# Kernel optimization log

Hardware: AMD Instinct MI355X
Metric: run time of the kernel (lower is better)

The kernel has to match this reference:

```python
import jax, jax.numpy as jnp
import numpy as np

D = 256      # d_model
A = 64       # attn_dim
K = 16       # k_neighbors
N = 20000    # embedding table rows
B = 32768    # batch of perturbed genes
SCALE = A ** -0.5
EPS = 1e-5


def setup_inputs() -> dict:
    key = jax.random.key(0)
    ks = jax.random.split(key, 12)
    all_embs = jax.random.normal(ks[0], (N, D), dtype=jnp.float32)
    center_idx = jax.random.randint(ks[1], (B,), 0, N)
    nb_idx = jax.random.randint(ks[2], (B, K), 0, N)
    nb_weights = jax.random.uniform(ks[3], (B, K), dtype=jnp.float32)
    # learned params (torch Linear weight layout: [out, in])
    s = lambda fan_in: 1.0 / np.sqrt(fan_in)
    Wq = jax.random.uniform(ks[4], (A, D), minval=-s(D), maxval=s(D))
    Wk = jax.random.uniform(ks[5], (A, D), minval=-s(D), maxval=s(D))
    Wg = jax.random.uniform(ks[6], (D, D), minval=-s(D), maxval=s(D))
    bg = jax.random.uniform(ks[7], (D,), minval=-s(D), maxval=s(D))
    Wo = jax.random.uniform(ks[8], (D, 2 * D), minval=-s(2 * D), maxval=s(2 * D))
    bo = jax.random.uniform(ks[9], (D,), minval=-s(2 * D), maxval=s(2 * D))
    gamma = jnp.ones((D,), jnp.float32)
    beta = jnp.zeros((D,), jnp.float32)
    return dict(all_embs=all_embs, center_idx=center_idx, nb_idx=nb_idx,
                nb_weights=nb_weights, Wq=Wq, Wk=Wk, Wg=Wg, bg=bg,
                Wo=Wo, bo=bo, gamma=gamma, beta=beta)


def reference(all_embs, center_idx, nb_idx, nb_weights, Wq, Wk, Wg, bg, Wo, bo, gamma, beta):
    center = all_embs[center_idx]                      # [B, D]
    nbs = all_embs[nb_idx]                             # [B, K, D]
    q = center @ Wq.T                                  # [B, A]
    k = jnp.einsum('bkd,ad->bka', nbs, Wk)             # [B, K, A]
    logits = jnp.einsum('ba,bka->bk', q, k) * SCALE
    logits = logits + jnp.log(jnp.clip(nb_weights, 1e-6))
    attn = jax.nn.softmax(logits, axis=-1)             # [B, K]
    gate = jax.nn.sigmoid(center @ Wg.T + bg)          # [B, D]
    context = gate * jnp.einsum('bk,bkd->bd', attn, nbs)
    combined = jnp.concatenate([center, context], axis=-1)  # [B, 2D]
    enriched = combined @ Wo.T + bo                    # [B, D]
    x = enriched + center
    mu = jnp.mean(x, axis=-1, keepdims=True)
    var = jnp.var(x, axis=-1, keepdims=True)
    return (x - mu) * jax.lax.rsqrt(var + EPS) * gamma + beta
```

## Files before the change

### kernel.cpp

```cpp
#include <hip/hip_runtime.h>

#define DD 256
#define MM 16

typedef __attribute__((ext_vector_type(8))) short bfrag;
typedef __attribute__((ext_vector_type(4))) float ffrag;

__device__ __forceinline__ float lo2f(unsigned int p){ union{unsigned int i; float f;} v; v.i = p<<16; return v.f; }
__device__ __forceinline__ float hi2f(unsigned int p){ union{unsigned int i; float f;} v; v.i = p & 0xffff0000u; return v.f; }
__device__ __forceinline__ float bf2f(unsigned short u){ union{unsigned int i; float f;} v; v.i = ((unsigned int)u)<<16; return v.f; }
__device__ __forceinline__ unsigned short f2b(float x){
    union{float f; unsigned int i;} v; v.f = x;
    unsigned int r = v.i + 0x7fffu + ((v.i>>16)&1u);
    return (unsigned short)(r>>16);
}
__device__ __forceinline__ unsigned int pack2(float a, float b){
    return (unsigned int)f2b(a) | ((unsigned int)f2b(b)<<16);
}

__device__ __forceinline__ int swz256(int d, int e){
    return ((d>>4)*8 + (e>>5))*512 + (((e>>3)&3)*16 + (d&15))*8 + (e&7);
}
__device__ __forceinline__ int swz512(int d, int e){
    return ((d>>4)*16 + (e>>5))*512 + (((e>>3)&3)*16 + (d&15))*8 + (e&7);
}

extern "C" __global__ __launch_bounds__(256)
void prep_all(const float* __restrict__ Wq, const float* __restrict__ Wk,
              const float* __restrict__ Wg, const float* __restrict__ Wo,
              const float* __restrict__ embs, unsigned short* __restrict__ ws, int n8)
{
    int bid = blockIdx.x, e = threadIdx.x;
    if (bid < 256) {
        int d = bid; float acc = 0.f;
        #pragma unroll 8
        for (int a = 0; a < 64; ++a) acc = fmaf(Wq[a*256 + e], Wk[a*256 + d], acc);
        ws[swz256(d, e)] = f2b(acc);
    } else if (bid < 512) {
        int r = bid - 256;
        ws[65536 + swz256(r, e)] = f2b(Wg[r*256 + e]);
    } else if (bid < 768) {
        int r = bid - 512;
        ws[131072 + swz512(r, e)]       = f2b(Wo[r*512 + e]);
        ws[131072 + swz512(r, e + 256)] = f2b(Wo[r*512 + 256 + e]);
    } else {
        int i = (bid - 768)*256 + e;
        if (i < n8) {
            const float4* s = (const float4*)embs + (size_t)i*2;
            float4 a = s[0], b = s[1];
            uint4 o;
            o.x = pack2(a.x,a.y); o.y = pack2(a.z,a.w);
            o.z = pack2(b.x,b.y); o.w = pack2(b.z,b.w);
            ((uint4*)(ws + 262144))[i] = o;
        }
    }
}

template<bool TBF>
__device__ __forceinline__ void gather8(uint4* buf, const unsigned short* tbl,
                                        const float* embs, int idx, int p)
{
    if (TBF) {
        const unsigned short* base = tbl + (size_t)idx*DD + p*8;
        #pragma unroll
        for (int i = 0; i < 8; ++i) buf[i] = *(const uint4*)(base + i*32);
    } else {
        const float* base = embs + (size_t)idx*DD + p*8;
        #pragma unroll
        for (int i = 0; i < 8; ++i) {
            float4 a = *(const float4*)(base + i*32);
            float4 b = *(const float4*)(base + i*32 + 4);
            buf[i].x = pack2(a.x,a.y); buf[i].y = pack2(a.z,a.w);
            buf[i].z = pack2(b.x,b.y); buf[i].w = pack2(b.z,b.w);
        }
    }
}

template<bool TBF>
__global__ __launch_bounds__(256, 3)
void na_mfma9(const float* __restrict__ embs,
              const int* __restrict__ cidx,
              const int* __restrict__ nidx,
              const float* __restrict__ nbw,
              const unsigned short* __restrict__ tbl,
              const unsigned short* __restrict__ wMt,
              const unsigned short* __restrict__ wWg,
              const unsigned short* __restrict__ wWo,
              const float* __restrict__ bg,
              const float* __restrict__ bo,
              const float* __restrict__ gamma,
              const float* __restrict__ beta,
              float* __restrict__ out)
{
    __shared__ __align__(16) unsigned short s_ax[16][264];
    __shared__ __align__(16) unsigned short s_t[16][264];
    __shared__ __align__(16) unsigned short s_nb[4][16][264];
    __shared__ float s_attn[4][16];
    __shared__ int   s_cidx[16];
    float* s_x = (float*)&s_nb[0][0][0];

    const int tid  = threadIdx.x;
    const int row0 = blockIdx.x * MM;
    const int lane = tid & 63, wv = tid >> 6;
    const int l15  = lane & 15, quad = lane >> 4;
    const ffrag fz = {0.f, 0.f, 0.f, 0.f};

    if (tid < 16) s_cidx[tid] = cidx[row0 + tid];
    uint4 careg[8];
    {
        int aidx = cidx[row0 + l15];
        if (TBF) {
            const unsigned short* pc = tbl + (size_t)aidx*DD + quad*8;
            #pragma unroll
            for (int kc = 0; kc < 8; ++kc) careg[kc] = *(const uint4*)(pc + kc*32);
        } else {
            const float* pc = embs + (size_t)aidx*DD + quad*8;
            #pragma unroll
            for (int kc = 0; kc < 8; ++kc) {
                float4 a = *(const float4*)(pc + kc*32);
                float4 b = *(const float4*)(pc + kc*32 + 4);
                careg[kc].x = pack2(a.x,a.y); careg[kc].y = pack2(a.z,a.w);
                careg[kc].z = pack2(b.x,b.y); careg[kc].w = pack2(b.z,b.w);
            }
        }
    }

    {
        ffrag at[4] = {fz,fz,fz,fz}, ag[4] = {fz,fz,fz,fz};
        const unsigned short* btA = wMt + (size_t)(wv*4)*4096 + lane*8;
        const unsigned short* bgA = wWg + (size_t)(wv*4)*4096 + lane*8;
        #pragma unroll
        for (int kc = 0; kc < 8; ++kc) {
            bfrag af = *(const bfrag*)&careg[kc];
            #pragma unroll
            for (int t = 0; t < 4; ++t) {
                at[t] = __builtin_amdgcn_mfma_f32_16x16x32_bf16(af, *(const bfrag*)(btA + (size_t)t*4096 + kc*512), at[t], 0,0,0);
                ag[t] = __builtin_amdgcn_mfma_f32_16x16x32_bf16(af, *(const bfrag*)(bgA + (size_t)t*4096 + kc*512), ag[t], 0,0,0);
            }
        }
        #pragma unroll
        for (int t = 0; t < 4; ++t) {
            int col = wv*64 + t*16 + l15;
            float bgv = bg[col];
            #pragma unroll
            for (int r = 0; r < 4; ++r) {
                int rr = quad*4 + r;
                s_t[rr][col]  = f2b(at[t][r]);
                float g = 1.f / (1.f + __expf(-(ag[t][r] + bgv)));
                s_ax[rr][col] = f2b(g);
            }
        }
    }
    __syncthreads();

    {
        const int kn = lane >> 2;
        const int p  = lane & 3;
        int idxs[4];
        #pragma unroll
        for (int j = 0; j < 4; ++j)
            idxs[j] = nidx[(size_t)(row0 + 4*wv + j) * 16 + kn];

        uint4 buf[2][8];
        gather8<TBF>(buf[0], tbl, embs, idxs[0], p);

        #pragma unroll
        for (int j = 0; j < 4; ++j) {
            if (j < 3) gather8<TBF>(buf[(j+1)&1], tbl, embs, idxs[j+1], p);
            const int m = 4*wv + j;
            unsigned short* nbp = &s_nb[wv][kn][p*8];
            #pragma unroll
            for (int i = 0; i < 8; ++i) *(uint4*)(nbp + i*32) = buf[j&1][i];

            const unsigned short* anb  = &s_nb[wv][l15][quad*8];
            const unsigned short* trow = &s_t[m][quad*8];
            ffrag lac = fz;
            #pragma unroll
            for (int kc = 0; kc < 8; ++kc)
                lac = __builtin_amdgcn_mfma_f32_16x16x32_bf16(
                        *(const bfrag*)(anb + kc*32), *(const bfrag*)(trow + kc*32), lac, 0,0,0);

            float4 w4 = *(const float4*)(nbw + (size_t)(row0 + m)*16 + quad*4);
            float lg0 = lac[0]*0.125f, lg1 = lac[1]*0.125f;
            float lg2 = lac[2]*0.125f, lg3 = lac[3]*0.125f;
            float mx = fmaxf(fmaxf(lg0, lg1), fmaxf(lg2, lg3));
            mx = fmaxf(mx, __shfl_xor(mx, 16));
            mx = fmaxf(mx, __shfl_xor(mx, 32));
            float e0 = fmaxf(w4.x, 1e-6f) * __expf(lg0 - mx);
            float e1 = fmaxf(w4.y, 1e-6f) * __expf(lg1 - mx);
            float e2 = fmaxf(w4.z, 1e-6f) * __expf(lg2 - mx);
            float e3 = fmaxf(w4.w, 1e-6f) * __expf(lg3 - mx);
            float s = e0 + e1 + e2 + e3;
            s += __shfl_xor(s, 16); s += __shfl_xor(s, 32);
            float inv = 1.f / s;
            if (l15 == 0)
                *(float4*)&s_attn[wv][quad*4] = make_float4(e0*inv, e1*inv, e2*inv, e3*inv);

            float4 aw0 = *(const float4*)&s_attn[wv][0];
            float4 aw1 = *(const float4*)&s_attn[wv][4];
            float4 aw2 = *(const float4*)&s_attn[wv][8];
            float4 aw3 = *(const float4*)&s_attn[wv][12];
            float aarr[16] = {aw0.x,aw0.y,aw0.z,aw0.w, aw1.x,aw1.y,aw1.z,aw1.w,
                              aw2.x,aw2.y,aw2.z,aw2.w, aw3.x,aw3.y,aw3.z,aw3.w};
            float c0=0.f, c1=0.f, c2=0.f, c3=0.f;
            #pragma unroll
            for (int kk = 0; kk < 16; ++kk) {
                uint2 v = *(const uint2*)&s_nb[wv][kk][lane*4];
                float a = aarr[kk];
                c0 += a * lo2f(v.x); c1 += a * hi2f(v.x);
                c2 += a * lo2f(v.y); c3 += a * hi2f(v.y);
            }
            uint2 g = *(const uint2*)&s_ax[m][lane*4];
            c0 *= lo2f(g.x); c1 *= hi2f(g.x); c2 *= lo2f(g.y); c3 *= hi2f(g.y);
            uint2 o; o.x = pack2(c0, c1); o.y = pack2(c2, c3);
            *(uint2*)&s_ax[m][lane*4] = o;
        }
    }
    __syncthreads();

    {
        ffrag acc[4] = {fz,fz,fz,fz};
        const unsigned short* arx = &s_ax[l15][quad * 8];
        const unsigned short* bO  = wWo + (size_t)(wv*4)*8192 + lane*8;
        #pragma unroll
        for (int kc = 0; kc < 8; ++kc) {
            bfrag af = *(const bfrag*)&careg[kc];
            #pragma unroll
            for (int t = 0; t < 4; ++t)
                acc[t] = __builtin_amdgcn_mfma_f32_16x16x32_bf16(af, *(const bfrag*)(bO + (size_t)t*8192 + kc*512), acc[t], 0,0,0);
        }
        #pragma unroll
        for (int kc = 8; kc < 16; ++kc) {
            bfrag af = *(const bfrag*)(arx + (kc-8)*32);
            #pragma unroll
            for (int t = 0; t < 4; ++t)
                acc[t] = __builtin_amdgcn_mfma_f32_16x16x32_bf16(af, *(const bfrag*)(bO + (size_t)t*8192 + kc*512), acc[t], 0,0,0);
        }
        #pragma unroll
        for (int t = 0; t < 4; ++t) {
            int col = wv*64 + t*16 + l15;
            float bov = bo[col];
            #pragma unroll
            for (int r = 0; r < 4; ++r) {
                int rr = quad*4 + r;
                float ctr = embs[(size_t)s_cidx[rr] * DD + col];
                s_x[rr*260 + col] = acc[t][r] + bov + ctr;
            }
        }
    }
    __syncthreads();

    {
        #pragma unroll
        for (int jj = 0; jj < 4; ++jj) {
            int m = wv * 4 + jj;
            const float* xr = s_x + m*260;
            float x0 = xr[lane],       x1 = xr[64 + lane];
            float x2 = xr[128 + lane], x3 = xr[192 + lane];
            float s  = x0 + x1 + x2 + x3;
            float ss = x0*x0 + x1*x1 + x2*x2 + x3*x3;
            #pragma unroll
            for (int off = 32; off >= 1; off >>= 1) {
                s  += __shfl_xor(s, off);
                ss += __shfl_xor(ss, off);
            }
            float mu  = s * (1.f/256.f);
            float var = ss * (1.f/256.f) - mu*mu;
            float rs  = rsqrtf(var + 1e-5f);
            size_t base = (size_t)(row0 + m) * DD;
            float xs[4] = {x0, x1, x2, x3};
            #pragma unroll
            for (int cc = 0; cc < 4; ++cc) {
                int dd = cc*64 + lane;
                out[base + dd] = (xs[cc] - mu) * rs * gamma[dd] + beta[dd];
            }
        }
    }
}

#define SD 260
#define KT 16
#define WS 17
extern "C" __global__ __launch_bounds__(256)
void na_f32_kernel(const float* __restrict__ embs, const int* __restrict__ center_idx,
                   const int* __restrict__ nb_idx, const float* __restrict__ nb_w,
                   const float* __restrict__ Wq, const float* __restrict__ Wk,
                   const float* __restrict__ Wg, const float* __restrict__ bg,
                   const float* __restrict__ Wo, const float* __restrict__ bo,
                   const float* __restrict__ gamma, const float* __restrict__ beta,
                   float* __restrict__ out)
{
    __shared__ __align__(16) float s_center[MM][SD];
    __shared__ __align__(16) float s_tc[MM][SD];
    __shared__ __align__(16) float s_nb[16][SD];
    __shared__ __align__(16) float s_w[DD][WS];
    __shared__ __align__(16) float s_q[MM][64];
    __shared__ float s_red[16][16];
    __shared__ float s_attn[16];
    const int tid = threadIdx.x;
    const int row0 = blockIdx.x * MM;
    const int td = tid & 63, tm = tid >> 6;
    {
        int m = tid >> 4, c = tid & 15;
        int idx = center_idx[row0 + m];
        const float4* src = (const float4*)(embs + (size_t)idx * DD) + c * 4;
        float4* dst = (float4*)&s_center[m][c * 16];
        dst[0]=src[0]; dst[1]=src[1]; dst[2]=src[2]; dst[3]=src[3];
    }
    __syncthreads();
    {
        const int a = tid & 63, mg = tid >> 6;
        float qacc[4] = {0,0,0,0};
        for (int kt = 0; kt < DD; kt += KT) {
            __syncthreads();
            { int r = tid >> 2, c4 = (tid & 3) * 4;
              *(float4*)&s_w[r][c4] = *(const float4*)(Wq + r * DD + kt + c4); }
            __syncthreads();
            #pragma unroll
            for (int kk = 0; kk < KT; kk += 4) {
                float4 b = *(const float4*)&s_w[a][kk];
                #pragma unroll
                for (int i = 0; i < 4; ++i) {
                    float4 av = *(const float4*)&s_center[4*mg + i][kt + kk];
                    qacc[i] += av.x*b.x + av.y*b.y + av.z*b.z + av.w*b.w;
                }
            }
        }
        __syncthreads();
        #pragma unroll
        for (int i = 0; i < 4; ++i) s_q[4*mg + i][a] = qacc[i];
    }
    __syncthreads();
    {
        float tacc[4][4];
        #pragma unroll
        for (int i=0;i<4;++i) { tacc[i][0]=tacc[i][1]=tacc[i][2]=tacc[i][3]=0.f; }
        for (int kk = 0; kk < 64; kk += 4) {
            float4 bk[4];
            #pragma unroll
            for (int t4 = 0; t4 < 4; ++t4)
                bk[t4] = *(const float4*)(Wk + (size_t)(kk + t4) * DD + 4 * td);
            #pragma unroll
            for (int i = 0; i < 4; ++i) {
                float4 av = *(const float4*)&s_q[4*tm + i][kk];
                tacc[i][0] += av.x*bk[0].x + av.y*bk[1].x + av.z*bk[2].x + av.w*bk[3].x;
                tacc[i][1] += av.x*bk[0].y + av.y*bk[1].y + av.z*bk[2].y + av.w*bk[3].y;
                tacc[i][2] += av.x*bk[0].z + av.y*bk[1].z + av.z*bk[2].z + av.w*bk[3].z;
                tacc[i][3] += av.x*bk[0].w + av.y*bk[1].w + av.z*bk[2].w + av.w*bk[3].w;
            }
        }
        #pragma unroll
        for (int i = 0; i < 4; ++i)
            *(float4*)&s_tc[4*tm + i][4*td] = make_float4(tacc[i][0],tacc[i][1],tacc[i][2],tacc[i][3]);
    }
    __syncthreads();
    for (int m = 0; m < MM; ++m) {
        { int k = tid >> 4, c = tid & 15;
          int idx = nb_idx[(row0 + m) * 16 + k];
          const float4* src = (const float4*)(embs + (size_t)idx * DD) + c * 4;
          float4* dst = (float4*)&s_nb[k][c * 16];
          dst[0]=src[0]; dst[1]=src[1]; dst[2]=src[2]; dst[3]=src[3]; }
        __syncthreads();
        { int k = tid >> 4, i = tid & 15;
          float acc = 0.f;
          #pragma unroll
          for (int j4 = 0; j4 < 4; ++j4) {
              float4 nv = *(const float4*)&s_nb[k][i*16 + 4*j4];
              float4 tv = *(const float4*)&s_tc[m][i*16 + 4*j4];
              acc += nv.x*tv.x + nv.y*tv.y + nv.z*tv.z + nv.w*tv.w;
          }
          s_red[k][i] = acc; }
        __syncthreads();
        if (tid < 16) {
            float lg = 0.f;
            #pragma unroll
            for (int i = 0; i < 16; ++i) lg += s_red[tid][i];
            float wv2 = nb_w[(row0 + m) * 16 + tid];
            lg = lg * 0.125f + logf(fmaxf(wv2, 1e-6f));
            float mx = lg;
            #pragma unroll
            for (int off = 8; off >= 1; off >>= 1) mx = fmaxf(mx, __shfl_xor(mx, off));
            float e = expf(lg - mx);
            float s = e;
            #pragma unroll
            for (int off = 8; off >= 1; off >>= 1) s += __shfl_xor(s, off);
            s_attn[tid] = e / s;
        }
        __syncthreads();
        { float acc = 0.f;
          #pragma unroll
          for (int k = 0; k < 16; ++k) acc += s_attn[k] * s_nb[k][tid];
          s_tc[m][tid] = acc; }
        __syncthreads();
    }
    {
        float acc[4][4];
        #pragma unroll
        for (int i=0;i<4;++i){acc[i][0]=acc[i][1]=acc[i][2]=acc[i][3]=0.f;}
        for (int kt = 0; kt < DD; kt += KT) {
            __syncthreads();
            #pragma unroll
            for (int j = 0; j < 4; ++j) {
                int r = (tid >> 2) + 64 * j, c4 = (tid & 3) * 4;
                *(float4*)&s_w[r][c4] = *(const float4*)(Wg + (size_t)r * DD + kt + c4);
            }
            __syncthreads();
            #pragma unroll
            for (int kk = 0; kk < KT; kk += 4) {
                float4 b[4];
                #pragma unroll
                for (int j = 0; j < 4; ++j) b[j] = *(const float4*)&s_w[4*td + j][kk];
                #pragma unroll
                for (int i = 0; i < 4; ++i) {
                    float4 av = *(const float4*)&s_center[4*tm + i][kt + kk];
                    #pragma unroll
                    for (int j = 0; j < 4; ++j)
                        acc[i][j] += av.x*b[j].x + av.y*b[j].y + av.z*b[j].z + av.w*b[j].w;
                }
            }
        }
        float bgv[4];
        #pragma unroll
        for (int j = 0; j < 4; ++j) bgv[j] = bg[4*td + j];
        __syncthreads();
        #pragma unroll
        for (int i = 0; i < 4; ++i)
            #pragma unroll
            for (int j = 0; j < 4; ++j) {
                float g = 1.f / (1.f + expf(-(acc[i][j] + bgv[j])));
                s_tc[4*tm + i][4*td + j] *= g;
            }
    }
    {
        float acc[4][4];
        #pragma unroll
        for (int i=0;i<4;++i){acc[i][0]=acc[i][1]=acc[i][2]=acc[i][3]=0.f;}
        for (int kt = 0; kt < 2*DD; kt += KT) {
            __syncthreads();
            #pragma unroll
            for (int j = 0; j < 4; ++j) {
                int r = (tid >> 2) + 64 * j, c4 = (tid & 3) * 4;
                *(float4*)&s_w[r][c4] = *(const float4*)(Wo + (size_t)r * 2 * DD + kt + c4);
            }
            __syncthreads();
            const float* Abase = (kt < DD) ? &s_center[0][0] : &s_tc[0][0];
            const int kb = (kt < DD) ? kt : kt - DD;
            #pragma unroll
            for (int kk = 0; kk < KT; kk += 4) {
                float4 b[4];
                #pragma unroll
                for (int j = 0; j < 4; ++j) b[j] = *(const float4*)&s_w[4*td + j][kk];
                #pragma unroll
                for (int i = 0; i < 4; ++i) {
                    float4 av = *(const float4*)(Abase + (4*tm + i) * SD + kb + kk);
                    #pragma unroll
                    for (int j = 0; j < 4; ++j)
                        acc[i][j] += av.x*b[j].x + av.y*b[j].y + av.z*b[j].z + av.w*b[j].w;
                }
            }
        }
        float bov[4];
        #pragma unroll
        for (int j = 0; j < 4; ++j) bov[j] = bo[4*td + j];
        __syncthreads();
        #pragma unroll
        for (int i = 0; i < 4; ++i)
            #pragma unroll
            for (int j = 0; j < 4; ++j)
                s_tc[4*tm + i][4*td + j] = acc[i][j] + bov[j] + s_center[4*tm + i][4*td + j];
    }
    __syncthreads();
    {
        int wv2 = tid >> 6, lane = tid & 63;
        #pragma unroll
        for (int jj = 0; jj < 4; ++jj) {
            int m = wv2 * 4 + jj;
            float x0 = s_tc[m][lane],       x1 = s_tc[m][64 + lane];
            float x2 = s_tc[m][128 + lane], x3 = s_tc[m][192 + lane];
            float s  = x0+x1+x2+x3;
            float ss = x0*x0 + x1*x1 + x2*x2 + x3*x3;
            #pragma unroll
            for (int off = 32; off >= 1; off >>= 1) { s += __shfl_xor(s, off); ss += __shfl_xor(ss, off); }
            float mu = s * (1.f/256.f);
            float var = ss * (1.f/256.f) - mu*mu;
            float rs = rsqrtf(var + 1e-5f);
            size_t base = (size_t)(row0 + m) * DD;
            float xs[4] = {x0,x1,x2,x3};
            #pragma unroll
            for (int c = 0; c < 4; ++c) {
                int dd = c*64 + lane;
                out[base + dd] = (xs[c] - mu) * rs * gamma[dd] + beta[dd];
            }
        }
    }
}

extern "C" void kernel_launch(void* const* d_in, const int* in_sizes, int n_in,
                              void* d_out, int out_size, void* d_ws, size_t ws_size,
                              hipStream_t stream) {
    const float* embs  = (const float*)d_in[0];
    const int*   cidx  = (const int*)d_in[1];
    const int*   nidx  = (const int*)d_in[2];
    const float* nbw   = (const float*)d_in[3];
    const float* Wq    = (const float*)d_in[4];
    const float* Wk    = (const float*)d_in[5];
    const float* Wg    = (const float*)d_in[6];
    const float* bg    = (const float*)d_in[7];
    const float* Wo    = (const float*)d_in[8];
    const float* bo    = (const float*)d_in[9];
    const float* gamma = (const float*)d_in[10];
    const float* beta  = (const float*)d_in[11];
    float* out = (float*)d_out;

    const int B = in_sizes[1];
    const int nemb = in_sizes[0];
    const size_t need_w = 262144 * 2;
    const size_t need_t = need_w + (size_t)nemb * 2;

    if (ws_size < need_w) {
        hipLaunchKernelGGL(na_f32_kernel, dim3(B / MM), dim3(256), 0, stream,
                           embs, cidx, nidx, nbw, Wq, Wk, Wg, bg, Wo, bo, gamma, beta, out);
        return;
    }
    unsigned short* wsb = (unsigned short*)d_ws;
    const bool use_tbl = (ws_size >= need_t) && ((nemb & 7) == 0);
    const int n8 = use_tbl ? (nemb / 8) : 0;
    const int prep_grid = 768 + (use_tbl ? (n8 + 255) / 256 : 0);
    hipLaunchKernelGGL(prep_all, dim3(prep_grid), dim3(256), 0, stream,
                       Wq, Wk, Wg, Wo, embs, wsb, n8);

    if (use_tbl) {
        hipLaunchKernelGGL(na_mfma9<true>, dim3(B / MM), dim3(256), 0, stream,
                           embs, cidx, nidx, nbw, wsb + 262144,
                           wsb, wsb + 65536, wsb + 131072,
                           bg, bo, gamma, beta, out);
    } else {
        hipLaunchKernelGGL(na_mfma9<false>, dim3(B / MM), dim3(256), 0, stream,
                           embs, cidx, nidx, nbw, (const unsigned short*)nullptr,
                           wsb, wsb + 65536, wsb + 131072,
                           bg, bo, gamma, beta, out);
    }
}
```

Measured before the change: 170.4 us.

## Halve neighbor LDS staging and compute attention logits with VALU dot products

Neighbor gathering is split into two halves of 8 neighbors, each lane holding 4 uint4 per neighbor. The logits come from per-lane VALU dot products against the projected query row with shuffle reductions, replacing the MFMA over a full 16-row LDS tile. LDS is restructured into a shared arena holding only 8 neighbor rows per wave, and launch bounds rise to 4 blocks per CU for higher occupancy. The trade is more VALU work, extra shuffles and reuse of the same LDS buffer for both halves, in exchange for a smaller LDS footprint and more blocks in flight to hide gather latency.

```diff
diff --git a/kernel.cpp b/kernel.cpp
--- a/kernel.cpp
+++ b/kernel.cpp
@@ -57,19 +57,19 @@
 }
 
 template<bool TBF>
-__device__ __forceinline__ void gather8(uint4* buf, const unsigned short* tbl,
-                                        const float* embs, int idx, int p)
+__device__ __forceinline__ void gather4(uint4* buf, const unsigned short* tbl,
+                                        const float* embs, int idx, int p8)
 {
     if (TBF) {
-        const unsigned short* base = tbl + (size_t)idx*DD + p*8;
-        #pragma unroll
-        for (int i = 0; i < 8; ++i) buf[i] = *(const uint4*)(base + i*32);
+        const unsigned short* base = tbl + (size_t)idx*DD + p8*8;
+        #pragma unroll
+        for (int i = 0; i < 4; ++i) buf[i] = *(const uint4*)(base + i*64);
     } else {
-        const float* base = embs + (size_t)idx*DD + p*8;
-        #pragma unroll
-        for (int i = 0; i < 8; ++i) {
-            float4 a = *(const float4*)(base + i*32);
-            float4 b = *(const float4*)(base + i*32 + 4);
+        const float* base = embs + (size_t)idx*DD + p8*8;
+        #pragma unroll
+        for (int i = 0; i < 4; ++i) {
+            float4 a = *(const float4*)(base + i*64);
+            float4 b = *(const float4*)(base + i*64 + 4);
             buf[i].x = pack2(a.x,a.y); buf[i].y = pack2(a.z,a.w);
             buf[i].z = pack2(b.x,b.y); buf[i].w = pack2(b.z,b.w);
         }
@@ -77,27 +77,29 @@
 }
 
 template<bool TBF>
-__global__ __launch_bounds__(256, 3)
-void na_mfma9(const float* __restrict__ embs,
-              const int* __restrict__ cidx,
-              const int* __restrict__ nidx,
-              const float* __restrict__ nbw,
-              const unsigned short* __restrict__ tbl,
-              const unsigned short* __restrict__ wMt,
-              const unsigned short* __restrict__ wWg,
-              const unsigned short* __restrict__ wWo,
-              const float* __restrict__ bg,
-              const float* __restrict__ bo,
-              const float* __restrict__ gamma,
-              const float* __restrict__ beta,
-              float* __restrict__ out)
+__global__ __launch_bounds__(256, 4)
+void na_mfma10(const float* __restrict__ embs,
+               const int* __restrict__ cidx,
+               const int* __restrict__ nidx,
+               const float* __restrict__ nbw,
+               const unsigned short* __restrict__ tbl,
+               const unsigned short* __restrict__ wMt,
+               const unsigned short* __restrict__ wWg,
+               const unsigned short* __restrict__ wWo,
+               const float* __restrict__ bg,
+               const float* __restrict__ bo,
+               const float* __restrict__ gamma,
+               const float* __restrict__ beta,
+               float* __restrict__ out)
 {
     __shared__ __align__(16) unsigned short s_ax[16][264];
-    __shared__ __align__(16) unsigned short s_t[16][264];
-    __shared__ __align__(16) unsigned short s_nb[4][16][264];
+    __shared__ __align__(16) unsigned short s_arena[12672];
     __shared__ float s_attn[4][16];
     __shared__ int   s_cidx[16];
-    float* s_x = (float*)&s_nb[0][0][0];
+
+    unsigned short (*s_t)[264]     = (unsigned short(*)[264])s_arena;
+    unsigned short (*s_nb)[8][264] = (unsigned short(*)[8][264])(s_arena + 4224);
+    float* s_x = (float*)s_arena;
 
     const int tid  = threadIdx.x;
     const int row0 = blockIdx.x * MM;
@@ -154,59 +156,81 @@
     __syncthreads();
 
     {
-        const int kn = lane >> 2;
-        const int p  = lane & 3;
-        int idxs[4];
-        #pragma unroll
-        for (int j = 0; j < 4; ++j)
-            idxs[j] = nidx[(size_t)(row0 + 4*wv + j) * 16 + kn];
-
-        uint4 buf[2][8];
-        gather8<TBF>(buf[0], tbl, embs, idxs[0], p);
-
+        const int kn2 = lane >> 3;
+        const int p8  = lane & 7;
+        int idxA[4], idxB[4];
         #pragma unroll
         for (int j = 0; j < 4; ++j) {
-            if (j < 3) gather8<TBF>(buf[(j+1)&1], tbl, embs, idxs[j+1], p);
+            idxA[j] = nidx[(size_t)(row0 + 4*wv + j) * 16 + kn2];
+            idxB[j] = nidx[(size_t)(row0 + 4*wv + j) * 16 + 8 + kn2];
+        }
+
+        uint4 bufA[2][4], bufB[4];
+        gather4<TBF>(bufA[0], tbl, embs, idxA[0], p8);
+
+        #pragma unroll
+        for (int j = 0; j < 4; ++j) {
             const int m = 4*wv + j;
-            unsigned short* nbp = &s_nb[wv][kn][p*8];
-            #pragma unroll
-            for (int i = 0; i < 8; ++i) *(uint4*)(nbp + i*32) = buf[j&1][i];
-
-            const unsigned short* anb  = &s_nb[wv][l15][quad*8];
-            const unsigned short* trow = &s_t[m][quad*8];
-            ffrag lac = fz;
-            #pragma unroll
-            for (int kc = 0; kc < 8; ++kc)
-                lac = __builtin_amdgcn_mfma_f32_16x16x32_bf16(
-                        *(const bfrag*)(anb + kc*32), *(const bfrag*)(trow + kc*32), lac, 0,0,0);
-
-            float4 w4 = *(const float4*)(nbw + (size_t)(row0 + m)*16 + quad*4);
-            float lg0 = lac[0]*0.125f, lg1 = lac[1]*0.125f;
-            float lg2 = lac[2]*0.125f, lg3 = lac[3]*0.125f;
-            float mx = fmaxf(fmaxf(lg0, lg1), fmaxf(lg2, lg3));
+            gather4<TBF>(bufB, tbl, embs, idxB[j], p8);
+
+            unsigned short* nbp = &s_nb[wv][kn2][p8*8];
+            #pragma unroll
+            for (int i = 0; i < 4; ++i) *(uint4*)(nbp + i*64) = bufA[j&1][i];
+
+            const unsigned short* trow = &s_t[m][p8*8];
+            float pA = 0.f, pB = 0.f;
+            #pragma unroll
+            for (int i = 0; i < 4; ++i) {
+                uint4 tv = *(const uint4*)(trow + i*64);
+                uint4 va = bufA[j&1][i];
+                pA += lo2f(va.x)*lo2f(tv.x) + hi2f(va.x)*hi2f(tv.x)
+                    + lo2f(va.y)*lo2f(tv.y) + hi2f(va.y)*hi2f(tv.y)
+                    + lo2f(va.z)*lo2f(tv.z) + hi2f(va.z)*hi2f(tv.z)
+                    + lo2f(va.w)*lo2f(tv.w) + hi2f(va.w)*hi2f(tv.w);
+                uint4 vb = bufB[i];
+                pB += lo2f(vb.x)*lo2f(tv.x) + hi2f(vb.x)*hi2f(tv.x)
+                    + lo2f(vb.y)*lo2f(tv.y) + hi2f(vb.y)*hi2f(tv.y)
+                    + lo2f(vb.z)*lo2f(tv.z) + hi2f(vb.z)*hi2f(tv.z)
+                    + lo2f(vb.w)*lo2f(tv.w) + hi2f(vb.w)*hi2f(tv.w);
+            }
+            pA += __shfl_xor(pA, 1); pA += __shfl_xor(pA, 2); pA += __shfl_xor(pA, 4);
+            pB += __shfl_xor(pB, 1); pB += __shfl_xor(pB, 2); pB += __shfl_xor(pB, 4);
+            float lgA = pA * 0.125f, lgB = pB * 0.125f;
+            float mx = fmaxf(lgA, lgB);
+            mx = fmaxf(mx, __shfl_xor(mx, 8));
             mx = fmaxf(mx, __shfl_xor(mx, 16));
             mx = fmaxf(mx, __shfl_xor(mx, 32));
-            float e0 = fmaxf(w4.x, 1e-6f) * __expf(lg0 - mx);
-            float e1 = fmaxf(w4.y, 1e-6f) * __expf(lg1 - mx);
-            float e2 = fmaxf(w4.z, 1e-6f) * __expf(lg2 - mx);
-            float e3 = fmaxf(w4.w, 1e-6f) * __expf(lg3 - mx);
-            float s = e0 + e1 + e2 + e3;
-            s += __shfl_xor(s, 16); s += __shfl_xor(s, 32);
+            float wA = fmaxf(nbw[(size_t)(row0 + m) * 16 + kn2],     1e-6f);
+            float wB = fmaxf(nbw[(size_t)(row0 + m) * 16 + 8 + kn2], 1e-6f);
+            float eA = wA * __expf(lgA - mx);
+            float eB = wB * __expf(lgB - mx);
+            float s = eA + eB;
+            s += __shfl_xor(s, 8); s += __shfl_xor(s, 16); s += __shfl_xor(s, 32);
             float inv = 1.f / s;
-            if (l15 == 0)
-                *(float4*)&s_attn[wv][quad*4] = make_float4(e0*inv, e1*inv, e2*inv, e3*inv);
+            if (p8 == 0) { s_attn[wv][kn2] = eA * inv; s_attn[wv][8 + kn2] = eB * inv; }
+
+            if (j < 3) gather4<TBF>(bufA[(j+1)&1], tbl, embs, idxA[j+1], p8);
 
             float4 aw0 = *(const float4*)&s_attn[wv][0];
             float4 aw1 = *(const float4*)&s_attn[wv][4];
+            float aarrA[8] = {aw0.x,aw0.y,aw0.z,aw0.w, aw1.x,aw1.y,aw1.z,aw1.w};
+            float c0=0.f, c1=0.f, c2=0.f, c3=0.f;
+            #pragma unroll
+            for (int kk = 0; kk < 8; ++kk) {
+                uint2 v = *(const uint2*)&s_nb[wv][kk][lane*4];
+                float a = aarrA[kk];
+                c0 += a * lo2f(v.x); c1 += a * hi2f(v.x);
+                c2 += a * lo2f(v.y); c3 += a * hi2f(v.y);
+            }
+            #pragma unroll
+            for (int i = 0; i < 4; ++i) *(uint4*)(nbp + i*64) = bufB[i];
             float4 aw2 = *(const float4*)&s_attn[wv][8];
             float4 aw3 = *(const float4*)&s_attn[wv][12];
-            float aarr[16] = {aw0.x,aw0.y,aw0.z,aw0.w, aw1.x,aw1.y,aw1.z,aw1.w,
-                              aw2.x,aw2.y,aw2.z,aw2.w, aw3.x,aw3.y,aw3.z,aw3.w};
-            float c0=0.f, c1=0.f, c2=0.f, c3=0.f;
-            #pragma unroll
-            for (int kk = 0; kk < 16; ++kk) {
+            float aarrB[8] = {aw2.x,aw2.y,aw2.z,aw2.w, aw3.x,aw3.y,aw3.z,aw3.w};
+            #pragma unroll
+            for (int kk = 0; kk < 8; ++kk) {
                 uint2 v = *(const uint2*)&s_nb[wv][kk][lane*4];
-                float a = aarr[kk];
+                float a = aarrB[kk];
                 c0 += a * lo2f(v.x); c1 += a * hi2f(v.x);
                 c2 += a * lo2f(v.y); c3 += a * hi2f(v.y);
             }
@@ -530,12 +554,12 @@
                        Wq, Wk, Wg, Wo, embs, wsb, n8);
 
     if (use_tbl) {
-        hipLaunchKernelGGL(na_mfma9<true>, dim3(B / MM), dim3(256), 0, stream,
+        hipLaunchKernelGGL(na_mfma10<true>, dim3(B / MM), dim3(256), 0, stream,
                            embs, cidx, nidx, nbw, wsb + 262144,
                            wsb, wsb + 65536, wsb + 131072,
                            bg, bo, gamma, beta, out);
     } else {
-        hipLaunchKernelGGL(na_mfma9<false>, dim3(B / MM), dim3(256), 0, stream,
+        hipLaunchKernelGGL(na_mfma10<false>, dim3(B / MM), dim3(256), 0, stream,
                            embs, cidx, nidx, nbw, (const unsigned short*)nullptr,
                            wsb, wsb + 65536, wsb + 131072,
                            bg, bo, gamma, beta, out);
```

Result: slower. 187.7 us (+10.2%).
